# Performance work log

Measured on AMD Instinct MI355X. Metric: run time of the kernel, lower is better.

The kernel has to match this reference:

```python
import jax, jax.numpy as jnp
import numpy as np

K = 3           # kernel_size
PAD = 1         # padding
HEADS = 6
C = 192
CH = C // HEADS           # channels per head = 32
SCALE = CH ** (-0.5)
KK = K * K                # 9


def unfold3(x):
    # x: [N,C,H,W] -> [N,C,9,H,W] (im2col with k=3, pad=1, stride=1)
    N, c, H, W = x.shape
    xp = jnp.pad(x, ((0, 0), (0, 0), (PAD, PAD), (PAD, PAD)))
    return jnp.stack([xp[:, :, i:i + H, j:j + W] for i in range(K) for j in range(K)], axis=2)


def fold3(y):
    # y: [N,C,9,H,W] -> [N,C,H,W] (scatter-add inverse of unfold3)
    N, c, kk, H, W = y.shape
    out = jnp.zeros((N, c, H + 2 * PAD, W + 2 * PAD), dtype=y.dtype)
    idx = 0
    for i in range(K):
        for j in range(K):
            out = out.at[:, :, i:i + H, j:j + W].add(y[:, :, idx])
            idx += 1
    return out[:, :, PAD:PAD + H, PAD:PAD + W]


def setup_inputs() -> dict:
    key = jax.random.key(0)
    ks = jax.random.split(key, 6)
    N, H, W = 16, 56, 56
    s = 0.02
    return {
        "x": jax.random.normal(ks[0], (N, C, H, W), jnp.float32),
        "Wv": jax.random.normal(ks[1], (C, C), jnp.float32) * s,          # fc (no bias)
        "Wa": jax.random.normal(ks[2], (C, KK * KK * HEADS), jnp.float32) * s,  # fc_att weight
        "ba": jax.random.normal(ks[3], (KK * KK * HEADS,), jnp.float32) * s,
        "Wp": jax.random.normal(ks[4], (C, C), jnp.float32) * s,          # fc_proj weight
        "bp": jax.random.normal(ks[5], (C,), jnp.float32) * s,
    }


def reference(x, Wv, Wa, ba, Wp, bp):
    N, c, H, W = x.shape
    HW = H * W
    # value projection (pointwise linear over channels)
    v = jnp.einsum("nchw,cd->ndhw", x, Wv)
    # unfold values: [N,C,9,H,W] -> [N,heads,ch,9,HW] -> [N,heads,HW,9,ch]
    vu = unfold3(v).reshape(N, HEADS, CH, KK, HW).transpose(0, 1, 4, 3, 2)
    # attention logits from (avg-pooled, here identity since stride=1) input
    att = jnp.einsum("nchw,ck->nhwk", x, Wa) + ba       # [N,H,W,81*heads]
    att = att.reshape(N, HW, HEADS, KK, KK).transpose(0, 2, 1, 3, 4)  # [N,heads,HW,9,9]
    att = jax.nn.softmax(att * SCALE, axis=-1)          # dropout is identity at inference
    # apply per-position 9x9 attention to the 9 gathered neighbors
    out = jnp.einsum("nhpkl,nhplc->nhpkc", att, vu)      # [N,heads,HW,9,ch]
    # fold back: layout (heads, ch, kk) matches unfold layout (C, kk)
    out = out.transpose(0, 1, 4, 3, 2).reshape(N, c, KK, H, W)
    folded = fold3(out)                                  # [N,C,H,W]
    # output projection
    return jnp.einsum("nchw,cd->ndhw", folded, Wp) + bp[None, :, None, None]
```

## Files before the change

kernel.cpp:

```cpp
#include <hip/hip_runtime.h>
#include <hip/hip_bf16.h>
#include <math.h>

#define HW 3136
#define NC 192
#define NHEADS 6
#define IMG 56
#define NATT 486
#define YSTR 768
#define ATT_SCALE 0.17677669529663687f

typedef __attribute__((ext_vector_type(8))) short short8;
typedef __attribute__((ext_vector_type(8))) unsigned short ushort8;
typedef __attribute__((ext_vector_type(4))) float float4v;

__device__ __forceinline__ float bf2f(unsigned short u) {
    unsigned int x = ((unsigned int)u) << 16;
    return __builtin_bit_cast(float, x);
}
__device__ __forceinline__ unsigned short f2bf(float f) {
    __hip_bfloat16 h = __float2bfloat16(f);
    return __builtin_bit_cast(unsigned short, h);
}
__device__ __forceinline__ void gload_lds16(const void* g, void* l) {
    __builtin_amdgcn_global_load_lds((const __attribute__((address_space(1))) void*)g,
                                     (__attribute__((address_space(3))) void*)l, 16, 0, 0);
}

__global__ __launch_bounds__(256) void transpose_x(const float* __restrict__ x,
                                                   unsigned short* __restrict__ xt)
{
    __shared__ float tile[64][65];
    int bx = blockIdx.x;
    int n = (bx * 64) / HW;
    int hw0 = (bx * 64) % HW;
    int c0 = blockIdx.y * 64;
    int tl = threadIdx.x & 63, tg = threadIdx.x >> 6;
    const float* xn = x + (size_t)n * NC * HW;
#pragma unroll
    for (int i = 0; i < 16; ++i)
        tile[tg * 16 + i][tl] = xn[(size_t)(c0 + tg * 16 + i) * HW + hw0 + tl];
    __syncthreads();
    unsigned short* xp = xt + ((size_t)n * HW + hw0) * NC + c0;
#pragma unroll
    for (int i = 0; i < 16; ++i) {
        int hwr = tg * 16 + i;
        xp[(size_t)hwr * NC + tl] = f2bf(tile[tl][hwr]);
    }
}

__global__ __launch_bounds__(256) void prep_weights(
    const float* __restrict__ Wv, const float* __restrict__ Wa, const float* __restrict__ Wp,
    const float* __restrict__ ba,
    unsigned short* __restrict__ Wall, unsigned short* __restrict__ Wpt,
    float* __restrict__ ball)
{
    int idx = blockIdx.x * 256 + threadIdx.x;
    if (idx < 36864) {
        int d = idx / 192, k = idx - d * 192;
        Wpt[idx] = f2bf(Wp[(size_t)k * NC + d]);
    }
    if (idx < 147456) {
        int d = idx / 192, k = idx - d * 192;
        unsigned short val;
        float bv = 0.f;
        if (d < 192) {
            val = f2bf(Wv[(size_t)k * NC + d]);
        } else {
            int dp = d - 192;
            int head = dp / 96, rr = dp - head * 96;
            int k9 = rr / 10, l = rr - k9 * 10;
            bool valid = (k9 < 9) && (l < 9);
            int src = head * 81 + k9 * 9 + l;
            val = valid ? f2bf(Wa[(size_t)k * NATT + src]) : (unsigned short)0;
            bv = valid ? ba[src] : 0.f;
        }
        Wall[idx] = val;
        if (k == 0) ball[d] = bv;
    }
}

__global__ __launch_bounds__(256) void gemm_big(
    const unsigned short* __restrict__ A, const unsigned short* __restrict__ W,
    const float* __restrict__ ball, unsigned short* __restrict__ Y)
{
    __shared__ __align__(16) unsigned short As[2][4096];
    __shared__ __align__(16) unsigned short Bs[2][4096];
    int t = threadIdx.x, lane = t & 63, wave = t >> 6;
    int col0 = blockIdx.x * 128, row0 = blockIdx.y * 128;
    int fr = lane & 15, fq = lane >> 4;
    int wm = (wave >> 1) * 64, wn = (wave & 1) * 64;
    int srow = lane >> 2;
    int soff = (lane & 3) * 16;
    const char* Ab = (const char*)A;
    const char* Wb = (const char*)W;

    float4v acc[4][4] = {};

#define STAGE_BIG(buf, k0)                                                        \
    {                                                                             \
        _Pragma("unroll")                                                         \
        for (int i = 0; i < 2; ++i) {                                             \
            int j = wave * 2 + i;                                                 \
            gload_lds16(Ab + (size_t)(row0 + j * 16 + srow) * 384 + (k0)*2 + soff,\
                        (char*)As[buf] + j * 1024);                               \
            gload_lds16(Wb + (size_t)(col0 + j * 16 + srow) * 384 + (k0)*2 + soff,\
                        (char*)Bs[buf] + j * 1024);                               \
        }                                                                         \
    }

    STAGE_BIG(0, 0);
    for (int s = 0; s < 6; ++s) {
        if (s < 5) STAGE_BIG((s + 1) & 1, (s + 1) * 32);
        __syncthreads();
        int buf = s & 1;
        short8 af[4], bf[4];
#pragma unroll
        for (int mi = 0; mi < 4; ++mi)
            af[mi] = *(const short8*)((const char*)As[buf] + (wm + mi * 16 + fr) * 64 + fq * 16);
#pragma unroll
        for (int ni = 0; ni < 4; ++ni)
            bf[ni] = *(const short8*)((const char*)Bs[buf] + (wn + ni * 16 + fr) * 64 + fq * 16);
#pragma unroll
        for (int mi = 0; mi < 4; ++mi)
#pragma unroll
            for (int ni = 0; ni < 4; ++ni)
                acc[mi][ni] = __builtin_amdgcn_mfma_f32_16x16x32_bf16(
                    af[mi], bf[ni], acc[mi][ni], 0, 0, 0);
        __syncthreads();
    }

#pragma unroll
    for (int ni = 0; ni < 4; ++ni) {
        int col = col0 + wn + ni * 16 + fr;
        float b = ball[col];
#pragma unroll
        for (int mi = 0; mi < 4; ++mi) {
            int row = row0 + wm + mi * 16 + fq * 4;
#pragma unroll
            for (int r = 0; r < 4; ++r)
                Y[(size_t)(row + r) * YSTR + col] = f2bf(acc[mi][ni][r] + b);
        }
    }
#undef STAGE_BIG
}

__global__ __launch_bounds__(256) void gemm_small(
    const unsigned short* __restrict__ A,
    const unsigned short* __restrict__ B,
    const float* __restrict__ bias, float* __restrict__ out)
{
    __shared__ __align__(16) unsigned short As[2][2048];
    __shared__ __align__(16) unsigned short Bs[2][8192];
    int t = threadIdx.x, lane = t & 63, wave = t >> 6;
    int n0 = blockIdx.x * 256, m0 = blockIdx.y * 64;
    int fr = lane & 15, fq = lane >> 4;
    int srow = lane >> 2, soff = (lane & 3) * 16;
    const char* Ab = (const char*)A;
    const char* Bb = (const char*)B;

    float4v acc[4][4] = {};

#define STAGE_SMALL(buf, k0)                                                      \
    {                                                                             \
        gload_lds16(Ab + (size_t)(m0 + wave * 16 + srow) * 384 + (k0)*2 + soff,   \
                    (char*)As[buf] + wave * 1024);                                \
        _Pragma("unroll")                                                         \
        for (int i = 0; i < 4; ++i) {                                             \
            int j = wave * 4 + i;                                                 \
            gload_lds16(Bb + (size_t)(n0 + j * 16 + srow) * 384 + (k0)*2 + soff,  \
                        (char*)Bs[buf] + j * 1024);                               \
        }                                                                         \
    }

    STAGE_SMALL(0, 0);
    for (int s = 0; s < 6; ++s) {
        if (s < 5) STAGE_SMALL((s + 1) & 1, (s + 1) * 32);
        __syncthreads();
        int buf = s & 1;
        short8 af[4], bf[4];
#pragma unroll
        for (int mi = 0; mi < 4; ++mi)
            af[mi] = *(const short8*)((const char*)As[buf] + (mi * 16 + fr) * 64 + fq * 16);
#pragma unroll
        for (int ni = 0; ni < 4; ++ni)
            bf[ni] = *(const short8*)((const char*)Bs[buf] + (wave * 64 + ni * 16 + fr) * 64 + fq * 16);
#pragma unroll
        for (int mi = 0; mi < 4; ++mi)
#pragma unroll
            for (int ni = 0; ni < 4; ++ni)
                acc[mi][ni] = __builtin_amdgcn_mfma_f32_16x16x32_bf16(
                    af[mi], bf[ni], acc[mi][ni], 0, 0, 0);
        __syncthreads();
    }

#pragma unroll
    for (int ni = 0; ni < 4; ++ni) {
        int n = n0 + wave * 64 + ni * 16 + fr;
        int img = n / HW, phw = n - img * HW;
        float* op = out + (size_t)img * (NC * HW) + phw;
#pragma unroll
        for (int mi = 0; mi < 4; ++mi) {
            int m = m0 + mi * 16 + fq * 4;
#pragma unroll
            for (int r = 0; r < 4; ++r)
                op[(size_t)(m + r) * HW] = acc[mi][ni][r] + bias[m + r];
        }
    }
#undef STAGE_SMALL
}

__global__ __launch_bounds__(256) void fused_att_agg(
    const unsigned short* __restrict__ Y, unsigned short* __restrict__ fold)
{
    __shared__ __align__(16) unsigned short vt[12 * 32 * 32];
    __shared__ float swc[224 * 25];
    int t = threadIdx.x;
    int bid = blockIdx.x;
    int head = bid % NHEADS; int tmp = bid / NHEADS;
    int tcol = tmp & 1; tmp >>= 1;
    int trow = tmp % 7; int img = tmp / 7;
    int h0 = trow * 8, w0 = tcol * 28;

    {
        const unsigned short* Yv = Y + head * 32;
#pragma unroll
        for (int i = 0; i < 6; ++i) {
            int u = i * 256 + t;
            int slot = u >> 2, q = u & 3;
            int vrow = slot >> 5, vcol = slot & 31;
            int hh = h0 - 2 + vrow, ww = w0 - 2 + vcol;
            bool ok = (hh >= 0) & (hh < IMG) & (ww >= 0) & (ww < IMG);
            ushort8 val = {};
            if (ok)
                val = *(const ushort8*)(Yv + (size_t)(img * HW + hh * IMG + ww) * YSTR + q * 8);
            *(ushort8*)&vt[(size_t)slot * 32 + q * 8] = val;
        }
    }

    if (t < 224) {
        int ph = t / 28, pw = t - (t / 28) * 28;
        int h = h0 + ph, w = w0 + pw;
        const unsigned short* attn =
            Y + (size_t)(img * HW + h * IMG + w) * YSTR + 192 + head * 96;
        float wc[25];
#pragma unroll
        for (int d = 0; d < 25; ++d) wc[d] = 0.f;
#pragma unroll
        for (int k = 0; k < 9; ++k) {
            const int oky = k / 3 - 1, okx = k % 3 - 1;
            int hh = h - oky, ww = w - okx;
            if (hh < 0 || hh >= IMG || ww < 0 || ww >= IMG) continue;
            const unsigned short* ap = attn - (ptrdiff_t)(oky * IMG + okx) * YSTR + k * 10;
            ushort8 a8;
            __builtin_memcpy(&a8, ap, 16);
            float a[9];
#pragma unroll
            for (int l = 0; l < 8; ++l) a[l] = bf2f(a8[l]);
            a[8] = bf2f(ap[8]);
            float m = -1e30f;
#pragma unroll
            for (int l = 0; l < 9; ++l) m = fmaxf(m, a[l]);
            float s = 0.f;
#pragma unroll
            for (int l = 0; l < 9; ++l) {
                a[l] = __expf((a[l] - m) * ATT_SCALE);
                s += a[l];
            }
            float r = 1.f / s;
#pragma unroll
            for (int l = 0; l < 9; ++l) {
                const int dy = (l / 3 - 1) - oky + 2;
                const int dx = (l % 3 - 1) - okx + 2;
                wc[dy * 5 + dx] += a[l] * r;
            }
        }
        float* o = swc + t * 25;
#pragma unroll
        for (int d = 0; d < 25; ++d) o[d] = wc[d];
    }
    __syncthreads();

#pragma unroll
    for (int i = 0; i < 4; ++i) {
        int item = i * 256 + t;
        if (item < 896) {
            int p = item >> 2, q8 = item & 3;
            int ph = p / 28, pw = p - (p / 28) * 28;
            const float* wp = swc + p * 25;
            float acc[8];
#pragma unroll
            for (int j = 0; j < 8; ++j) acc[j] = 0.f;
#pragma unroll
            for (int d = 0; d < 25; ++d) {
                const int dy = d / 5, dx = d % 5;
                float wf = wp[d];
                ushort8 vv = *(const ushort8*)&vt[(((ph + dy) << 5) + (pw + dx)) * 32 + q8 * 8];
#pragma unroll
                for (int j = 0; j < 8; ++j)
                    acc[j] += wf * bf2f(vv[j]);
            }
            int rem = img * HW + (h0 + ph) * IMG + (w0 + pw);
            unsigned short* fo = fold + (size_t)rem * NC + head * 32 + q8 * 8;
            ushort8 ov;
#pragma unroll
            for (int j = 0; j < 8; ++j) ov[j] = f2bf(acc[j]);
            *(ushort8*)fo = ov;
        }
    }
}

extern "C" void kernel_launch(void* const* d_in, const int* in_sizes, int n_in,
                              void* d_out, int out_size, void* d_ws, size_t ws_size,
                              hipStream_t stream)
{
    const float* x  = (const float*)d_in[0];
    const float* Wv = (const float*)d_in[1];
    const float* Wa = (const float*)d_in[2];
    const float* ba = (const float*)d_in[3];
    const float* Wp = (const float*)d_in[4];
    const float* bp = (const float*)d_in[5];
    float* out = (float*)d_out;

    unsigned short* xt    = (unsigned short*)d_ws;
    unsigned short* Y     = xt + 9633792;
    unsigned short* Wall  = Y + 38535168;
    unsigned short* Wpt   = Wall + 147456;
    float*          ball  = (float*)(Wpt + 36864);
    unsigned short* foldb = xt;

    dim3 blk(256);
    prep_weights<<<576, blk, 0, stream>>>(Wv, Wa, Wp, ba, Wall, Wpt, ball);
    transpose_x<<<dim3(784, 3), blk, 0, stream>>>(x, xt);
    gemm_big<<<dim3(6, 392), blk, 0, stream>>>(xt, Wall, ball, Y);
    fused_att_agg<<<1344, blk, 0, stream>>>(Y, foldb);
    gemm_small<<<dim3(196, 3), blk, 0, stream>>>(Wpt, foldb, bp, out);
}
```

Baseline: 194.9 us.

## Fuse x transpose/bf16 cast into value-attention GEMM and store softmax weights as bf16

Removes the separate transpose_x kernel: gemm_big now reads fp32 x directly in NCHW layout, converts it to bf16 and writes it transposed into LDS. The GEMM tile is reshaped to 64 rows by 256 columns so each block re-reads the A tile across only 3 column blocks. The combined per-position 5x5 weights in the attention kernel are also stored in LDS as bf16 instead of fp32 to cut shared memory use. This trades an extra global round trip for strided fp32 loads in the GEMM, and adds some precision loss on the aggregation weights.

```diff
diff --git a/kernel.cpp b/kernel.cpp
--- a/kernel.cpp
+++ b/kernel.cpp
@@ -25,28 +25,6 @@
 __device__ __forceinline__ void gload_lds16(const void* g, void* l) {
     __builtin_amdgcn_global_load_lds((const __attribute__((address_space(1))) void*)g,
                                      (__attribute__((address_space(3))) void*)l, 16, 0, 0);
-}
-
-__global__ __launch_bounds__(256) void transpose_x(const float* __restrict__ x,
-                                                   unsigned short* __restrict__ xt)
-{
-    __shared__ float tile[64][65];
-    int bx = blockIdx.x;
-    int n = (bx * 64) / HW;
-    int hw0 = (bx * 64) % HW;
-    int c0 = blockIdx.y * 64;
-    int tl = threadIdx.x & 63, tg = threadIdx.x >> 6;
-    const float* xn = x + (size_t)n * NC * HW;
-#pragma unroll
-    for (int i = 0; i < 16; ++i)
-        tile[tg * 16 + i][tl] = xn[(size_t)(c0 + tg * 16 + i) * HW + hw0 + tl];
-    __syncthreads();
-    unsigned short* xp = xt + ((size_t)n * HW + hw0) * NC + c0;
-#pragma unroll
-    for (int i = 0; i < 16; ++i) {
-        int hwr = tg * 16 + i;
-        xp[(size_t)hwr * NC + tl] = f2bf(tile[tl][hwr]);
-    }
 }
 
 __global__ __launch_bounds__(256) void prep_weights(
@@ -81,46 +59,55 @@
 }
 
 __global__ __launch_bounds__(256) void gemm_big(
-    const unsigned short* __restrict__ A, const unsigned short* __restrict__ W,
+    const float* __restrict__ x, const unsigned short* __restrict__ W,
     const float* __restrict__ ball, unsigned short* __restrict__ Y)
 {
-    __shared__ __align__(16) unsigned short As[2][4096];
-    __shared__ __align__(16) unsigned short Bs[2][4096];
+    __shared__ __align__(16) unsigned short As[2][64 * 32];
+    __shared__ __align__(16) unsigned short Bs[2][256 * 32];
     int t = threadIdx.x, lane = t & 63, wave = t >> 6;
-    int col0 = blockIdx.x * 128, row0 = blockIdx.y * 128;
+    int col0 = blockIdx.x * 256;
+    int row0 = blockIdx.y * 64;
+    int img = row0 / HW, hw0 = row0 % HW;
+    const float* xb = x + (size_t)img * (NC * HW) + hw0;
+
     int fr = lane & 15, fq = lane >> 4;
-    int wm = (wave >> 1) * 64, wn = (wave & 1) * 64;
-    int srow = lane >> 2;
-    int soff = (lane & 3) * 16;
-    const char* Ab = (const char*)A;
+    int ar = t & 63;
+    int ak = t >> 6;
+    int srow = lane >> 2, soff = (lane & 3) * 16;
     const char* Wb = (const char*)W;
 
     float4v acc[4][4] = {};
 
-#define STAGE_BIG(buf, k0)                                                        \
+#define STAGE(buf, k0)                                                            \
     {                                                                             \
+        float av[8];                                                              \
         _Pragma("unroll")                                                         \
-        for (int i = 0; i < 2; ++i) {                                             \
-            int j = wave * 2 + i;                                                 \
-            gload_lds16(Ab + (size_t)(row0 + j * 16 + srow) * 384 + (k0)*2 + soff,\
-                        (char*)As[buf] + j * 1024);                               \
+        for (int j = 0; j < 8; ++j)                                               \
+            av[j] = xb[(size_t)((k0) + ak * 8 + j) * HW + ar];                    \
+        ushort8 ab;                                                               \
+        _Pragma("unroll")                                                         \
+        for (int j = 0; j < 8; ++j) ab[j] = f2bf(av[j]);                          \
+        *(ushort8*)&As[buf][ar * 32 + ak * 8] = ab;                               \
+        _Pragma("unroll")                                                         \
+        for (int i = 0; i < 4; ++i) {                                             \
+            int j = wave * 4 + i;                                                 \
             gload_lds16(Wb + (size_t)(col0 + j * 16 + srow) * 384 + (k0)*2 + soff,\
                         (char*)Bs[buf] + j * 1024);                               \
         }                                                                         \
     }
 
-    STAGE_BIG(0, 0);
+    STAGE(0, 0);
     for (int s = 0; s < 6; ++s) {
-        if (s < 5) STAGE_BIG((s + 1) & 1, (s + 1) * 32);
+        if (s < 5) STAGE((s + 1) & 1, (s + 1) * 32);
         __syncthreads();
         int buf = s & 1;
         short8 af[4], bf[4];
 #pragma unroll
         for (int mi = 0; mi < 4; ++mi)
-            af[mi] = *(const short8*)((const char*)As[buf] + (wm + mi * 16 + fr) * 64 + fq * 16);
+            af[mi] = *(const short8*)&As[buf][(mi * 16 + fr) * 32 + fq * 8];
 #pragma unroll
         for (int ni = 0; ni < 4; ++ni)
-            bf[ni] = *(const short8*)((const char*)Bs[buf] + (wn + ni * 16 + fr) * 64 + fq * 16);
+            bf[ni] = *(const short8*)&Bs[buf][(wave * 64 + ni * 16 + fr) * 32 + fq * 8];
 #pragma unroll
         for (int mi = 0; mi < 4; ++mi)
 #pragma unroll
@@ -132,17 +119,17 @@
 
 #pragma unroll
     for (int ni = 0; ni < 4; ++ni) {
-        int col = col0 + wn + ni * 16 + fr;
+        int col = col0 + wave * 64 + ni * 16 + fr;
         float b = ball[col];
 #pragma unroll
         for (int mi = 0; mi < 4; ++mi) {
-            int row = row0 + wm + mi * 16 + fq * 4;
+            int row = row0 + mi * 16 + fq * 4;
 #pragma unroll
             for (int r = 0; r < 4; ++r)
                 Y[(size_t)(row + r) * YSTR + col] = f2bf(acc[mi][ni][r] + b);
         }
     }
-#undef STAGE_BIG
+#undef STAGE
 }
 
 __global__ __launch_bounds__(256) void gemm_small(
@@ -214,7 +201,7 @@
     const unsigned short* __restrict__ Y, unsigned short* __restrict__ fold)
 {
     __shared__ __align__(16) unsigned short vt[12 * 32 * 32];
-    __shared__ float swc[224 * 25];
+    __shared__ unsigned short swc[224 * 25];
     int t = threadIdx.x;
     int bid = blockIdx.x;
     int head = bid % NHEADS; int tmp = bid / NHEADS;
@@ -275,9 +262,9 @@
                 wc[dy * 5 + dx] += a[l] * r;
             }
         }
-        float* o = swc + t * 25;
-#pragma unroll
-        for (int d = 0; d < 25; ++d) o[d] = wc[d];
+        unsigned short* o = swc + t * 25;
+#pragma unroll
+        for (int d = 0; d < 25; ++d) o[d] = f2bf(wc[d]);
     }
     __syncthreads();
 
@@ -287,14 +274,14 @@
         if (item < 896) {
             int p = item >> 2, q8 = item & 3;
             int ph = p / 28, pw = p - (p / 28) * 28;
-            const float* wp = swc + p * 25;
+            const unsigned short* wp = swc + p * 25;
             float acc[8];
 #pragma unroll
             for (int j = 0; j < 8; ++j) acc[j] = 0.f;
 #pragma unroll
             for (int d = 0; d < 25; ++d) {
                 const int dy = d / 5, dx = d % 5;
-                float wf = wp[d];
+                float wf = bf2f(wp[d]);
                 ushort8 vv = *(const ushort8*)&vt[(((ph + dy) << 5) + (pw + dx)) * 32 + q8 * 8];
 #pragma unroll
                 for (int j = 0; j < 8; ++j)
@@ -322,17 +309,15 @@
     const float* bp = (const float*)d_in[5];
     float* out = (float*)d_out;
 
-    unsigned short* xt    = (unsigned short*)d_ws;
-    unsigned short* Y     = xt + 9633792;
+    unsigned short* foldb = (unsigned short*)d_ws;
+    unsigned short* Y     = foldb + 9633792;
     unsigned short* Wall  = Y + 38535168;
     unsigned short* Wpt   = Wall + 147456;
     float*          ball  = (float*)(Wpt + 36864);
-    unsigned short* foldb = xt;
 
     dim3 blk(256);
     prep_weights<<<576, blk, 0, stream>>>(Wv, Wa, Wp, ba, Wall, Wpt, ball);
-    transpose_x<<<dim3(784, 3), blk, 0, stream>>>(x, xt);
-    gemm_big<<<dim3(6, 392), blk, 0, stream>>>(xt, Wall, ball, Y);
+    gemm_big<<<dim3(3, 784), blk, 0, stream>>>(x, Wall, ball, Y);
     fused_att_agg<<<1344, blk, 0, stream>>>(Y, foldb);
     gemm_small<<<dim3(196, 3), blk, 0, stream>>>(Wpt, foldb, bp, out);
 }
```

Measured after the change: 198.2 us. No clear change (+1.7%).
